# Optimization experiments

Measured on AMD Instinct MI355X. Metric: run time of the kernel, lower is better.

The kernel has to match this reference:

```python
import jax, jax.numpy as jnp
import numpy as np

NUM_HEADS = 8
NEG_INF = float(-2**32 + 1)
LN_EPS = 1e-8


def setup_inputs() -> dict:
    key = jax.random.key(0)
    ks = jax.random.split(key, 9)
    B, T, D = 4, 2048, 512
    inp = {
        "queries": jax.random.normal(ks[0], (B, T, D), jnp.float32),
        "keys": jax.random.normal(ks[1], (B, T, D), jnp.float32),
        "values": jax.random.normal(ks[2], (B, T, D), jnp.float32),
        "Wq": jax.random.normal(ks[3], (D, D), jnp.float32) / np.sqrt(D),
        "bq": jnp.zeros((D,), jnp.float32),
        "Wk": jax.random.normal(ks[4], (D, D), jnp.float32) / np.sqrt(D),
        "bk": jnp.zeros((D,), jnp.float32),
        "Wv": jax.random.normal(ks[5], (D, D), jnp.float32) / np.sqrt(D),
        "bv": jnp.zeros((D,), jnp.float32),
        "gamma": jnp.ones((D,), jnp.float32),
        "beta": jnp.zeros((D,), jnp.float32),
    }
    return inp


def _split_heads(x, h):
    # torch.cat(torch.chunk(x, h, dim=2), dim=0): [B,T,D] -> [h*B, T, D/h], head-major
    B, T, D = x.shape
    return x.reshape(B, T, h, D // h).transpose(2, 0, 1, 3).reshape(h * B, T, D // h)


def _merge_heads(x, h, B):
    # inverse: [h*B, T, dh] -> [B, T, h*dh]
    hB, T, dh = x.shape
    return x.reshape(h, B, T, dh).transpose(1, 2, 0, 3).reshape(B, T, h * dh)


def reference(queries, keys, values, Wq, bq, Wk, bk, Wv, bv, gamma, beta):
    h = NUM_HEADS
    B, Tq, D = queries.shape
    dh = D // h

    Q = jax.nn.relu(queries @ Wq + bq)
    K = jax.nn.relu(keys @ Wk + bk)
    V = jax.nn.relu(values @ Wv + bv)

    Q_ = _split_heads(Q, h)  # [h*B, Tq, dh]
    K_ = _split_heads(K, h)
    V_ = _split_heads(V, h)

    scores = jnp.einsum('bqd,bkd->bqk', Q_, K_) / jnp.sqrt(jnp.float32(dh))  # [h*B, Tq, Tk]

    # key padding mask: zero rows in `keys` get -inf scores
    key_mask = jnp.sign(jnp.abs(jnp.sum(keys, axis=-1)))  # [B, Tk]
    key_mask = jnp.tile(key_mask, (h, 1))  # [h*B, Tk]
    scores = jnp.where(key_mask[:, None, :] == 0.0, NEG_INF, scores)

    attn = jax.nn.softmax(scores, axis=-1)

    # query mask applied multiplicatively post-softmax
    query_mask = jnp.sign(jnp.abs(jnp.sum(queries, axis=-1)))  # [B, Tq]
    query_mask = jnp.tile(query_mask, (h, 1))  # [h*B, Tq]
    attn = attn * query_mask[:, :, None]

    out = jnp.einsum('bqk,bkd->bqd', attn, V_)  # [h*B, Tq, dh]
    out = _merge_heads(out, h, B) + queries  # residual

    # custom LayerNorm: torch.std is unbiased (ddof=1), eps added to std
    mean = out.mean(-1, keepdims=True)
    std = jnp.sqrt(out.var(-1, ddof=1, keepdims=True))
    return gamma * (out - mean) / (std + LN_EPS) + beta
```

## Files before the change

kernel.cpp:

```cpp
#include <hip/hip_runtime.h>


typedef __attribute__((ext_vector_type(8))) __bf16 bf16x8;
typedef __attribute__((ext_vector_type(4))) float f32x4;

#if __has_builtin(__builtin_amdgcn_exp2f)
#define EXP2F __builtin_amdgcn_exp2f
#else
#define EXP2F exp2f
#endif

#define QSCALE (0.125f * 1.4426950408889634f)

__device__ __forceinline__ unsigned short f2bf(float f) {
  return __builtin_bit_cast(unsigned short, (__bf16)f);
}
__device__ __forceinline__ unsigned pk2(float a, float b) {
  return (unsigned)f2bf(a) | ((unsigned)f2bf(b) << 16);
}
__device__ __forceinline__ f32x4 mfma16(bf16x8 a, bf16x8 b, f32x4 c) {
  return __builtin_amdgcn_mfma_f32_16x16x32_bf16(a, b, c, 0, 0, 0);
}
__device__ __forceinline__ bf16x8 ld_bf8(const unsigned short* p) {
  return *(const bf16x8*)p;
}
__device__ __forceinline__ void g2l16(const void* g, void* l) {
  __builtin_amdgcn_global_load_lds(
      (const __attribute__((address_space(1))) void*)g,
      (__attribute__((address_space(3))) void*)l, 16, 0, 0);
}

__global__ __launch_bounds__(256) void wt_kernel(const float* __restrict__ Wq,
                                                 const float* __restrict__ Wk,
                                                 const float* __restrict__ Wv,
                                                 unsigned short* __restrict__ Wt) {
  int idx = blockIdx.x * 256 + threadIdx.x;
  int o = idx * 8;
  int z = o >> 18;
  int rem = o & 262143;
  int n = rem >> 9;
  int k0 = rem & 511;
  const float* W = (z == 0) ? Wq : ((z == 1) ? Wk : Wv);
  unsigned int w[4];
#pragma unroll
  for (int i = 0; i < 4; ++i) {
    unsigned short lo = f2bf(W[(k0 + 2 * i) * 512 + n]);
    unsigned short hi = f2bf(W[(k0 + 2 * i + 1) * 512 + n]);
    w[i] = (unsigned)lo | ((unsigned)hi << 16);
  }
  *(uint4*)(Wt + o) = make_uint4(w[0], w[1], w[2], w[3]);
}

__global__ __launch_bounds__(256, 3) void proj_kernel(
    const float* __restrict__ Xq, const float* __restrict__ Xk,
    const float* __restrict__ Xv, const float* __restrict__ bq,
    const float* __restrict__ bk, const float* __restrict__ bv,
    const unsigned short* __restrict__ Wt, unsigned short* __restrict__ Qb,
    unsigned short* __restrict__ Kb, unsigned short* __restrict__ Vt,
    float* __restrict__ qmask, float* __restrict__ kbias) {
  __shared__ float Asm[128][32];
  __shared__ unsigned short Bsm[128][32];

  int tid = threadIdx.x;
  int m0g = blockIdx.x * 128;
  int z = m0g >> 13;
  int m0 = m0g & 8191;
  int n0 = blockIdx.y * 128;
  const float* X = (z == 0) ? Xq : ((z == 1) ? Xk : Xv);
  const float* bias = (z == 0) ? bq : ((z == 1) ? bk : bv);
  const unsigned short* Wz = Wt + z * 262144;

  int w = tid >> 6, lane = tid & 63;
  int wm = w >> 1, wn = w & 1;
  int mrow = lane & 15, quad = lane >> 4;
  int m7 = mrow & 7;

  int arow = tid >> 3, aslot = tid & 7;
  const float* gA = X + (m0 + arow) * 512 + ((aslot ^ (arow & 7)) * 4);
  char* lA = (char*)&Asm[0][0] + tid * 16;

  int srow = tid >> 2, schk = tid & 3;
  const unsigned short* gB = Wz + (n0 + srow) * 512 + schk * 8;
  char* lB = (char*)&Bsm[0][0] + tid * 16;

  const unsigned short* rB = &Bsm[0][quad * 8];

  f32x4 zero = {0.f, 0.f, 0.f, 0.f};
  f32x4 acc[4][4];
#pragma unroll
  for (int i = 0; i < 4; ++i)
#pragma unroll
    for (int j = 0; j < 4; ++j) acc[i][j] = zero;

  bool domask = (z < 2) && (n0 == 0) && (wn == 0);
  float rsum[4] = {0.f, 0.f, 0.f, 0.f};

  for (int kc = 0; kc < 16; ++kc) {
    int ko = kc * 32;
#pragma unroll
    for (int j = 0; j < 4; ++j) g2l16(gA + ko + j * 32 * 512, lA + j * 4096);
    g2l16(gB + ko, lB);
    g2l16(gB + ko + 64 * 512, lB + 4096);
    __syncthreads();

    bf16x8 af[4], bfr[4];
#pragma unroll
    for (int mt = 0; mt < 4; ++mt) {
      const float* pa = &Asm[wm * 64 + mt * 16 + mrow][0];
      f32x4 lo = *(const f32x4*)(pa + ((2 * quad) ^ m7) * 4);
      f32x4 hi = *(const f32x4*)(pa + ((2 * quad + 1) ^ m7) * 4);
      if (domask)
        rsum[mt] += lo[0] + lo[1] + lo[2] + lo[3] + hi[0] + hi[1] + hi[2] + hi[3];
      bf16x8 t;
      t[0] = (__bf16)lo[0]; t[1] = (__bf16)lo[1];
      t[2] = (__bf16)lo[2]; t[3] = (__bf16)lo[3];
      t[4] = (__bf16)hi[0]; t[5] = (__bf16)hi[1];
      t[6] = (__bf16)hi[2]; t[7] = (__bf16)hi[3];
      af[mt] = t;
    }
#pragma unroll
    for (int nt = 0; nt < 4; ++nt)
      bfr[nt] = ld_bf8(rB + (wn * 64 + nt * 16 + mrow) * 32);
#pragma unroll
    for (int mt = 0; mt < 4; ++mt)
#pragma unroll
      for (int nt = 0; nt < 4; ++nt)
        acc[mt][nt] = mfma16(af[mt], bfr[nt], acc[mt][nt]);
    __syncthreads();
  }

  if (domask) {
    float* msk = (z == 0) ? qmask : kbias;
#pragma unroll
    for (int mt = 0; mt < 4; ++mt) {
      float s = rsum[mt];
      s += __shfl_xor(s, 16);
      s += __shfl_xor(s, 32);
      if (quad == 0) {
        float v;
        if (z == 0)
          v = (s == 0.f) ? 0.f : 1.f;
        else
          v = (s == 0.f) ? -1.0e30f : 0.f;
        msk[m0 + wm * 64 + mt * 16 + mrow] = v;
      }
    }
  }

  if (z < 2) {
    unsigned short* dst = (z == 0) ? Qb : Kb;
    float sc = (z == 0) ? QSCALE : 1.0f;
#pragma unroll
    for (int nt = 0; nt < 4; ++nt) {
      int n = n0 + wn * 64 + nt * 16 + mrow;
      float bv_ = bias[n];
#pragma unroll
      for (int mt = 0; mt < 4; ++mt) {
        int m = m0 + wm * 64 + mt * 16 + quad * 4;
#pragma unroll
        for (int r = 0; r < 4; ++r) {
          float v = fmaxf(acc[mt][nt][r] + bv_, 0.f) * sc;
          dst[(m + r) * 512 + n] = f2bf(v);
        }
      }
    }
  } else {
#pragma unroll
    for (int nt = 0; nt < 4; ++nt) {
      int n = n0 + wn * 64 + nt * 16 + mrow;
      int hh = n >> 6, jj = n & 63;
      float bv_ = bias[n];
#pragma unroll
      for (int mt = 0; mt < 4; ++mt) {
        int grow = m0 + wm * 64 + mt * 16 + quad * 4;
        int bb = grow >> 11, tl = grow & 2047;
        int pos = (tl & ~31) + quad * 8 + (mt & 1) * 4;
        float p0 = fmaxf(acc[mt][nt][0] + bv_, 0.f);
        float p1 = fmaxf(acc[mt][nt][1] + bv_, 0.f);
        float p2 = fmaxf(acc[mt][nt][2] + bv_, 0.f);
        float p3 = fmaxf(acc[mt][nt][3] + bv_, 0.f);
        *(uint2*)(Vt + ((hh * 4 + bb) * 64 + jj) * 2048 + pos) =
            make_uint2(pk2(p0, p1), pk2(p2, p3));
      }
    }
  }
}

__global__ __launch_bounds__(512, 4) void attn_kernel(
    const unsigned short* __restrict__ Qb, const unsigned short* __restrict__ Kb,
    const unsigned short* __restrict__ Vt, const float* __restrict__ qmask,
    const float* __restrict__ kbias, const float* __restrict__ queries,
    float* __restrict__ out) {
  __shared__ char smem[66560];
  unsigned short* KsmS = (unsigned short*)smem;
  unsigned short* VsmS = (unsigned short*)(smem + 32768);
  float* Obuf = (float*)smem;
  float* lbuf = (float*)(smem + 65536);

  int hb = blockIdx.x;
  int qt = blockIdx.y;
  int h = hb >> 2, b = hb & 3;
  int q0 = qt * 128;
  int tid = threadIdx.x;
  int w = tid >> 6, lane = tid & 63;
  int qh = w >> 1, kh2 = w & 1;
  int mrow = lane & 15, quad = lane >> 4;

  const unsigned short* gK =
      Kb + (b * 2048 + (tid >> 3)) * 512 + h * 64 + (((tid & 7) ^ ((tid >> 3) & 7)) * 8);
  const unsigned short* gV =
      Vt + (hb * 64 + (tid >> 4)) * 2048 + (((tid & 15) ^ ((tid >> 4) & 15)) * 8);

  bf16x8 qf[2][2];
  {
    const unsigned short* qp =
        Qb + (b * 2048 + q0 + qh * 32 + mrow) * 512 + h * 64 + quad * 8;
#pragma unroll
    for (int qn = 0; qn < 2; ++qn) {
      qf[qn][0] = ld_bf8(qp + qn * 8192);
      qf[qn][1] = ld_bf8(qp + qn * 8192 + 32);
    }
  }

  bf16x8 onev;
#pragma unroll
  for (int i = 0; i < 8; ++i) onev[i] = (__bf16)1.0f;

  f32x4 zero = {0.f, 0.f, 0.f, 0.f};
  f32x4 oacc[4][2];
#pragma unroll
  for (int i = 0; i < 4; ++i)
#pragma unroll
    for (int j = 0; j < 2; ++j) oacc[i][j] = zero;
  f32x4 lacc[2] = {zero, zero};

  const float* kmB = kbias + b * 2048 + kh2 * 64 + quad * 4;
  const int kfrow = kh2 * 64;
  const int mlow = mrow & 7;

#pragma unroll
  for (int j = 0; j < 2; ++j) {
    g2l16(gK + j * 64 * 512, &KsmS[j * 4096 + tid * 8]);
    g2l16(gV + j * 32 * 2048, &VsmS[j * 4096 + tid * 8]);
  }

  for (int it = 0; it < 16; ++it) {
    int bi = it & 1;
    int kb = it * 128;
    __syncthreads();

    if (it < 15) {
      int nkb = kb + 128;
      int nb = 1 - bi;
#pragma unroll
      for (int j = 0; j < 2; ++j) {
        g2l16(gK + (nkb + j * 64) * 512, &KsmS[nb * 8192 + j * 4096 + tid * 8]);
        g2l16(gV + nkb + j * 32 * 2048, &VsmS[nb * 8192 + j * 4096 + tid * 8]);
      }
    }

    f32x4 kmv[4];
#pragma unroll
    for (int mt = 0; mt < 4; ++mt)
      kmv[mt] = *(const f32x4*)(kmB + kb + mt * 16);

#pragma unroll
    for (int kg = 0; kg < 2; ++kg) {
      bf16x8 kfA0 = ld_bf8(&KsmS[bi * 8192 + (kfrow + kg * 32 + mrow) * 64 +
                                 ((quad) ^ mlow) * 8]);
      bf16x8 kfA1 = ld_bf8(&KsmS[bi * 8192 + (kfrow + kg * 32 + mrow) * 64 +
                                 ((4 + quad) ^ mlow) * 8]);
      bf16x8 kfB0 = ld_bf8(&KsmS[bi * 8192 + (kfrow + kg * 32 + 16 + mrow) * 64 +
                                 ((quad) ^ mlow) * 8]);
      bf16x8 kfB1 = ld_bf8(&KsmS[bi * 8192 + (kfrow + kg * 32 + 16 + mrow) * 64 +
                                 ((4 + quad) ^ mlow) * 8]);
      bf16x8 vfg[4];
#pragma unroll
      for (int dt = 0; dt < 4; ++dt)
        vfg[dt] = ld_bf8(&VsmS[bi * 8192 + (dt * 16 + mrow) * 128 +
                               ((kh2 * 8 + kg * 4 + quad) ^ mrow) * 8]);

      f32x4 sA[2], sB[2];
#pragma unroll
      for (int qn = 0; qn < 2; ++qn) {
        f32x4 s0 = mfma16(kfA0, qf[qn][0], kmv[kg * 2]);
        sA[qn] = mfma16(kfA1, qf[qn][1], s0);
        f32x4 s1 = mfma16(kfB0, qf[qn][0], kmv[kg * 2 + 1]);
        sB[qn] = mfma16(kfB1, qf[qn][1], s1);
      }
#pragma unroll
      for (int qn = 0; qn < 2; ++qn) {
        f32x4 p0, p1;
#pragma unroll
        for (int r = 0; r < 4; ++r) {
          p0[r] = EXP2F(sA[qn][r]);
          p1[r] = EXP2F(sB[qn][r]);
        }
        bf16x8 pf = __builtin_bit_cast(
            bf16x8, make_uint4(pk2(p0[0], p0[1]), pk2(p0[2], p0[3]),
                               pk2(p1[0], p1[1]), pk2(p1[2], p1[3])));
        lacc[qn] = mfma16(pf, onev, lacc[qn]);
#pragma unroll
        for (int dt = 0; dt < 4; ++dt)
          oacc[dt][qn] = mfma16(pf, vfg[dt], oacc[dt][qn]);
      }
    }
  }

  __syncthreads();
  if (mrow == 0) {
#pragma unroll
    for (int qn = 0; qn < 2; ++qn)
#pragma unroll
      for (int r = 0; r < 4; ++r)
        lbuf[kh2 * 128 + qh * 32 + qn * 16 + quad * 4 + r] = lacc[qn][r];
  }
  if (kh2 == 1) {
#pragma unroll
    for (int dt = 0; dt < 4; ++dt)
#pragma unroll
      for (int qn = 0; qn < 2; ++qn)
#pragma unroll
        for (int r = 0; r < 4; ++r)
          Obuf[(qh * 32 + qn * 16 + quad * 4 + r) * 65 + dt * 16 + mrow] =
              oacc[dt][qn][r];
  }
  __syncthreads();
  if (kh2 == 0) {
#pragma unroll
    for (int qn = 0; qn < 2; ++qn) {
#pragma unroll
      for (int r = 0; r < 4; ++r) {
        int qrow = qh * 32 + qn * 16 + quad * 4 + r;
        float l = lbuf[qrow] + lbuf[128 + qrow];
        int qg = b * 2048 + q0 + qrow;
        float inv = qmask[qg] / l;
#pragma unroll
        for (int dt = 0; dt < 4; ++dt) {
          int idx = qg * 512 + h * 64 + dt * 16 + mrow;
          out[idx] =
              (oacc[dt][qn][r] + Obuf[qrow * 65 + dt * 16 + mrow]) * inv +
              queries[idx];
        }
      }
    }
  }
}

__global__ __launch_bounds__(256) void ln_kernel(float* __restrict__ out,
                                                 const float* __restrict__ gamma,
                                                 const float* __restrict__ beta) {
  int row = blockIdx.x * 4 + (threadIdx.x >> 6);
  int lane = threadIdx.x & 63;
  float* p = out + row * 512;
  float4 v1 = ((const float4*)p)[lane];
  float4 v2 = ((const float4*)p)[64 + lane];
  float s = v1.x + v1.y + v1.z + v1.w + v2.x + v2.y + v2.z + v2.w;
  float sq = v1.x * v1.x + v1.y * v1.y + v1.z * v1.z + v1.w * v1.w +
             v2.x * v2.x + v2.y * v2.y + v2.z * v2.z + v2.w * v2.w;
#pragma unroll
  for (int off = 32; off > 0; off >>= 1) {
    s += __shfl_xor(s, off);
    sq += __shfl_xor(sq, off);
  }
  float mean = s * (1.f / 512.f);
  float var = fmaxf((sq - 512.f * mean * mean) * (1.f / 511.f), 0.f);
  float inv = 1.f / (sqrtf(var) + 1e-8f);
  float4 g1 = ((const float4*)gamma)[lane];
  float4 g2 = ((const float4*)gamma)[64 + lane];
  float4 b1 = ((const float4*)beta)[lane];
  float4 b2 = ((const float4*)beta)[64 + lane];
  v1.x = g1.x * (v1.x - mean) * inv + b1.x;
  v1.y = g1.y * (v1.y - mean) * inv + b1.y;
  v1.z = g1.z * (v1.z - mean) * inv + b1.z;
  v1.w = g1.w * (v1.w - mean) * inv + b1.w;
  v2.x = g2.x * (v2.x - mean) * inv + b2.x;
  v2.y = g2.y * (v2.y - mean) * inv + b2.y;
  v2.z = g2.z * (v2.z - mean) * inv + b2.z;
  v2.w = g2.w * (v2.w - mean) * inv + b2.w;
  ((float4*)p)[lane] = v1;
  ((float4*)p)[64 + lane] = v2;
}

extern "C" void kernel_launch(void* const* d_in, const int* in_sizes, int n_in,
                              void* d_out, int out_size, void* d_ws, size_t ws_size,
                              hipStream_t stream) {
  (void)in_sizes; (void)n_in; (void)out_size; (void)ws_size;
  const float* queries = (const float*)d_in[0];
  const float* keys    = (const float*)d_in[1];
  const float* values  = (const float*)d_in[2];
  const float* Wq = (const float*)d_in[3];
  const float* bq = (const float*)d_in[4];
  const float* Wk = (const float*)d_in[5];
  const float* bk = (const float*)d_in[6];
  const float* Wv = (const float*)d_in[7];
  const float* bv = (const float*)d_in[8];
  const float* gamma = (const float*)d_in[9];
  const float* beta  = (const float*)d_in[10];
  float* out = (float*)d_out;

  char* ws = (char*)d_ws;
  unsigned short* Qb = (unsigned short*)(ws);
  unsigned short* Kb = (unsigned short*)(ws + 8 * 1024 * 1024);
  unsigned short* Vt = (unsigned short*)(ws + 16 * 1024 * 1024);
  unsigned short* Wt = (unsigned short*)(ws + 24 * 1024 * 1024);
  float* qmask = (float*)(ws + 24 * 1024 * 1024 + 3 * 512 * 512 * 2);
  float* kbias = qmask + 8192;

  wt_kernel<<<384, 256, 0, stream>>>(Wq, Wk, Wv, Wt);
  proj_kernel<<<dim3(192, 4), 256, 0, stream>>>(queries, keys, values, bq, bk, bv,
                                                Wt, Qb, Kb, Vt, qmask, kbias);
  attn_kernel<<<dim3(32, 16), 512, 0, stream>>>(Qb, Kb, Vt, qmask, kbias, queries, out);
  ln_kernel<<<2048, 256, 0, stream>>>(out, gamma, beta);
}
```

Before: 193.4 us.

## Pre-convert inputs to bf16, double-buffer projection GEMM, shrink attention tiles

Adds a separate kernel that converts the Q/K/V inputs to bf16 and computes the query and key masks, so the projection GEMM loads bf16 tiles with double-buffered LDS prefetch and no longer converts or reduces per tile. The attention kernel moves to 256 threads and 64 query rows per block, doubling the grid. It reads V fragments straight from global memory instead of staging them in LDS, and replaces the ones-vector MFMA row-sum with scalar adds plus shuffles. The trade-offs are an extra kernel launch and an extra round trip of the inputs through memory (partly staged in the output buffer), plus uncoalesced global V loads in the inner loop.

```diff
diff --git a/kernel.cpp b/kernel.cpp
--- a/kernel.cpp
+++ b/kernel.cpp
@@ -51,39 +51,66 @@
   *(uint4*)(Wt + o) = make_uint4(w[0], w[1], w[2], w[3]);
 }
 
-__global__ __launch_bounds__(256, 3) void proj_kernel(
+__global__ __launch_bounds__(256) void xcvt_kernel(
     const float* __restrict__ Xq, const float* __restrict__ Xk,
-    const float* __restrict__ Xv, const float* __restrict__ bq,
+    const float* __restrict__ Xv, unsigned short* __restrict__ Xbq,
+    unsigned short* __restrict__ Xbk, unsigned short* __restrict__ Xbv,
+    float* __restrict__ qmask, float* __restrict__ kbias) {
+  int row = blockIdx.x * 4 + (threadIdx.x >> 6);
+  int lane = threadIdx.x & 63;
+  int z = row >> 13;
+  int r = row & 8191;
+  const float* X = (z == 0) ? Xq : ((z == 1) ? Xk : Xv);
+  unsigned short* Xb = (z == 0) ? Xbq : ((z == 1) ? Xbk : Xbv);
+  const float* p = X + r * 512 + lane * 8;
+  f32x4 lo = *(const f32x4*)p;
+  f32x4 hi = *(const f32x4*)(p + 4);
+  *(uint4*)(Xb + r * 512 + lane * 8) =
+      make_uint4(pk2(lo[0], lo[1]), pk2(lo[2], lo[3]), pk2(hi[0], hi[1]),
+                 pk2(hi[2], hi[3]));
+  if (z < 2) {
+    float s = lo[0] + lo[1] + lo[2] + lo[3] + hi[0] + hi[1] + hi[2] + hi[3];
+#pragma unroll
+    for (int off = 1; off < 64; off <<= 1) s += __shfl_xor(s, off);
+    if (lane == 0) {
+      if (z == 0)
+        qmask[r] = (s == 0.f) ? 0.f : 1.f;
+      else
+        kbias[r] = (s == 0.f) ? -1.0e30f : 0.f;
+    }
+  }
+}
+
+__global__ __launch_bounds__(256, 4) void proj_kernel(
+    const unsigned short* __restrict__ Xbq, const unsigned short* __restrict__ Xbk,
+    const unsigned short* __restrict__ Xbv, const float* __restrict__ bq,
     const float* __restrict__ bk, const float* __restrict__ bv,
     const unsigned short* __restrict__ Wt, unsigned short* __restrict__ Qb,
-    unsigned short* __restrict__ Kb, unsigned short* __restrict__ Vt,
-    float* __restrict__ qmask, float* __restrict__ kbias) {
-  __shared__ float Asm[128][32];
-  __shared__ unsigned short Bsm[128][32];
+    unsigned short* __restrict__ Kb, unsigned short* __restrict__ Vt) {
+  __shared__ unsigned short Asm[2][128][32];
+  __shared__ unsigned short Bsm[2][128][32];
 
   int tid = threadIdx.x;
   int m0g = blockIdx.x * 128;
   int z = m0g >> 13;
   int m0 = m0g & 8191;
   int n0 = blockIdx.y * 128;
-  const float* X = (z == 0) ? Xq : ((z == 1) ? Xk : Xv);
+  const unsigned short* Xb = (z == 0) ? Xbq : ((z == 1) ? Xbk : Xbv);
   const float* bias = (z == 0) ? bq : ((z == 1) ? bk : bv);
   const unsigned short* Wz = Wt + z * 262144;
 
   int w = tid >> 6, lane = tid & 63;
   int wm = w >> 1, wn = w & 1;
   int mrow = lane & 15, quad = lane >> 4;
-  int m7 = mrow & 7;
-
-  int arow = tid >> 3, aslot = tid & 7;
-  const float* gA = X + (m0 + arow) * 512 + ((aslot ^ (arow & 7)) * 4);
-  char* lA = (char*)&Asm[0][0] + tid * 16;
-
-  int srow = tid >> 2, schk = tid & 3;
-  const unsigned short* gB = Wz + (n0 + srow) * 512 + schk * 8;
-  char* lB = (char*)&Bsm[0][0] + tid * 16;
-
-  const unsigned short* rB = &Bsm[0][quad * 8];
+
+  int srow = tid >> 2, sslot = tid & 3;
+  int sxs = sslot ^ ((srow >> 1) & 3);
+  const unsigned short* gA = Xb + (m0 + srow) * 512 + sxs * 8;
+  const unsigned short* gB = Wz + (n0 + srow) * 512 + sxs * 8;
+  char* lA = (char*)&Asm[0][0][0] + tid * 16;
+  char* lB = (char*)&Bsm[0][0][0] + tid * 16;
+
+  int rs = (quad ^ ((mrow >> 1) & 3)) * 8;
 
   f32x4 zero = {0.f, 0.f, 0.f, 0.f};
   f32x4 acc[4][4];
@@ -92,59 +119,35 @@
 #pragma unroll
     for (int j = 0; j < 4; ++j) acc[i][j] = zero;
 
-  bool domask = (z < 2) && (n0 == 0) && (wn == 0);
-  float rsum[4] = {0.f, 0.f, 0.f, 0.f};
+  g2l16(gA, lA);
+  g2l16(gA + 64 * 512, lA + 4096);
+  g2l16(gB, lB);
+  g2l16(gB + 64 * 512, lB + 4096);
+  __syncthreads();
 
   for (int kc = 0; kc < 16; ++kc) {
-    int ko = kc * 32;
-#pragma unroll
-    for (int j = 0; j < 4; ++j) g2l16(gA + ko + j * 32 * 512, lA + j * 4096);
-    g2l16(gB + ko, lB);
-    g2l16(gB + ko + 64 * 512, lB + 4096);
-    __syncthreads();
-
+    int cur = kc & 1;
+    if (kc < 15) {
+      int ko = (kc + 1) * 32;
+      int nb = cur ^ 1;
+      g2l16(gA + ko, lA + nb * 8192);
+      g2l16(gA + ko + 64 * 512, lA + nb * 8192 + 4096);
+      g2l16(gB + ko, lB + nb * 8192);
+      g2l16(gB + ko + 64 * 512, lB + nb * 8192 + 4096);
+    }
     bf16x8 af[4], bfr[4];
 #pragma unroll
-    for (int mt = 0; mt < 4; ++mt) {
-      const float* pa = &Asm[wm * 64 + mt * 16 + mrow][0];
-      f32x4 lo = *(const f32x4*)(pa + ((2 * quad) ^ m7) * 4);
-      f32x4 hi = *(const f32x4*)(pa + ((2 * quad + 1) ^ m7) * 4);
-      if (domask)
-        rsum[mt] += lo[0] + lo[1] + lo[2] + lo[3] + hi[0] + hi[1] + hi[2] + hi[3];
-      bf16x8 t;
-      t[0] = (__bf16)lo[0]; t[1] = (__bf16)lo[1];
-      t[2] = (__bf16)lo[2]; t[3] = (__bf16)lo[3];
-      t[4] = (__bf16)hi[0]; t[5] = (__bf16)hi[1];
-      t[6] = (__bf16)hi[2]; t[7] = (__bf16)hi[3];
-      af[mt] = t;
-    }
+    for (int mt = 0; mt < 4; ++mt)
+      af[mt] = ld_bf8(&Asm[cur][wm * 64 + mt * 16 + mrow][rs]);
 #pragma unroll
     for (int nt = 0; nt < 4; ++nt)
-      bfr[nt] = ld_bf8(rB + (wn * 64 + nt * 16 + mrow) * 32);
+      bfr[nt] = ld_bf8(&Bsm[cur][wn * 64 + nt * 16 + mrow][rs]);
 #pragma unroll
     for (int mt = 0; mt < 4; ++mt)
 #pragma unroll
       for (int nt = 0; nt < 4; ++nt)
         acc[mt][nt] = mfma16(af[mt], bfr[nt], acc[mt][nt]);
     __syncthreads();
-  }
-
-  if (domask) {
-    float* msk = (z == 0) ? qmask : kbias;
-#pragma unroll
-    for (int mt = 0; mt < 4; ++mt) {
-      float s = rsum[mt];
-      s += __shfl_xor(s, 16);
-      s += __shfl_xor(s, 32);
-      if (quad == 0) {
-        float v;
-        if (z == 0)
-          v = (s == 0.f) ? 0.f : 1.f;
-        else
-          v = (s == 0.f) ? -1.0e30f : 0.f;
-        msk[m0 + wm * 64 + mt * 16 + mrow] = v;
-      }
-    }
   }
 
   if (z < 2) {
@@ -186,30 +189,30 @@
   }
 }
 
-__global__ __launch_bounds__(512, 4) void attn_kernel(
+__global__ __launch_bounds__(256, 4) void attn_kernel(
     const unsigned short* __restrict__ Qb, const unsigned short* __restrict__ Kb,
     const unsigned short* __restrict__ Vt, const float* __restrict__ qmask,
     const float* __restrict__ kbias, const float* __restrict__ queries,
     float* __restrict__ out) {
-  __shared__ char smem[66560];
+  __shared__ char smem[33280];
   unsigned short* KsmS = (unsigned short*)smem;
-  unsigned short* VsmS = (unsigned short*)(smem + 32768);
   float* Obuf = (float*)smem;
-  float* lbuf = (float*)(smem + 65536);
+  float* lbuf = (float*)(smem + 32768);
 
   int hb = blockIdx.x;
   int qt = blockIdx.y;
   int h = hb >> 2, b = hb & 3;
-  int q0 = qt * 128;
+  int q0 = qt * 64;
   int tid = threadIdx.x;
   int w = tid >> 6, lane = tid & 63;
   int qh = w >> 1, kh2 = w & 1;
   int mrow = lane & 15, quad = lane >> 4;
+  int mlow = mrow & 7;
 
   const unsigned short* gK =
       Kb + (b * 2048 + (tid >> 3)) * 512 + h * 64 + (((tid & 7) ^ ((tid >> 3) & 7)) * 8);
   const unsigned short* gV =
-      Vt + (hb * 64 + (tid >> 4)) * 2048 + (((tid & 15) ^ ((tid >> 4) & 15)) * 8);
+      Vt + (hb * 64 + mrow) * 2048 + (kh2 * 8 + quad) * 8;
 
   bf16x8 qf[2][2];
   {
@@ -222,27 +225,20 @@
     }
   }
 
-  bf16x8 onev;
-#pragma unroll
-  for (int i = 0; i < 8; ++i) onev[i] = (__bf16)1.0f;
-
   f32x4 zero = {0.f, 0.f, 0.f, 0.f};
   f32x4 oacc[4][2];
 #pragma unroll
   for (int i = 0; i < 4; ++i)
 #pragma unroll
     for (int j = 0; j < 2; ++j) oacc[i][j] = zero;
-  f32x4 lacc[2] = {zero, zero};
+  float lpart[2] = {0.f, 0.f};
 
   const float* kmB = kbias + b * 2048 + kh2 * 64 + quad * 4;
   const int kfrow = kh2 * 64;
-  const int mlow = mrow & 7;
-
-#pragma unroll
-  for (int j = 0; j < 2; ++j) {
-    g2l16(gK + j * 64 * 512, &KsmS[j * 4096 + tid * 8]);
-    g2l16(gV + j * 32 * 2048, &VsmS[j * 4096 + tid * 8]);
-  }
+
+#pragma unroll
+  for (int j = 0; j < 4; ++j)
+    g2l16(gK + j * 32 * 512, &KsmS[j * 2048 + tid * 8]);
 
   for (int it = 0; it < 16; ++it) {
     int bi = it & 1;
@@ -250,22 +246,16 @@
     __syncthreads();
 
     if (it < 15) {
-      int nkb = kb + 128;
       int nb = 1 - bi;
 #pragma unroll
-      for (int j = 0; j < 2; ++j) {
-        g2l16(gK + (nkb + j * 64) * 512, &KsmS[nb * 8192 + j * 4096 + tid * 8]);
-        g2l16(gV + nkb + j * 32 * 2048, &VsmS[nb * 8192 + j * 4096 + tid * 8]);
-      }
-    }
-
-    f32x4 kmv[4];
-#pragma unroll
-    for (int mt = 0; mt < 4; ++mt)
-      kmv[mt] = *(const f32x4*)(kmB + kb + mt * 16);
+      for (int j = 0; j < 4; ++j)
+        g2l16(gK + (kb + 128 + j * 32) * 512, &KsmS[nb * 8192 + j * 2048 + tid * 8]);
+    }
 
 #pragma unroll
     for (int kg = 0; kg < 2; ++kg) {
+      f32x4 km0 = *(const f32x4*)(kmB + kb + kg * 32);
+      f32x4 km1 = *(const f32x4*)(kmB + kb + kg * 32 + 16);
       bf16x8 kfA0 = ld_bf8(&KsmS[bi * 8192 + (kfrow + kg * 32 + mrow) * 64 +
                                  ((quad) ^ mlow) * 8]);
       bf16x8 kfA1 = ld_bf8(&KsmS[bi * 8192 + (kfrow + kg * 32 + mrow) * 64 +
@@ -277,15 +267,14 @@
       bf16x8 vfg[4];
 #pragma unroll
       for (int dt = 0; dt < 4; ++dt)
-        vfg[dt] = ld_bf8(&VsmS[bi * 8192 + (dt * 16 + mrow) * 128 +
-                               ((kh2 * 8 + kg * 4 + quad) ^ mrow) * 8]);
+        vfg[dt] = ld_bf8(gV + dt * 16 * 2048 + kb + kg * 32);
 
       f32x4 sA[2], sB[2];
 #pragma unroll
       for (int qn = 0; qn < 2; ++qn) {
-        f32x4 s0 = mfma16(kfA0, qf[qn][0], kmv[kg * 2]);
+        f32x4 s0 = mfma16(kfA0, qf[qn][0], km0);
         sA[qn] = mfma16(kfA1, qf[qn][1], s0);
-        f32x4 s1 = mfma16(kfB0, qf[qn][0], kmv[kg * 2 + 1]);
+        f32x4 s1 = mfma16(kfB0, qf[qn][0], km1);
         sB[qn] = mfma16(kfB1, qf[qn][1], s1);
       }
 #pragma unroll
@@ -296,10 +285,10 @@
           p0[r] = EXP2F(sA[qn][r]);
           p1[r] = EXP2F(sB[qn][r]);
         }
+        lpart[qn] += p0[0] + p0[1] + p0[2] + p0[3] + p1[0] + p1[1] + p1[2] + p1[3];
         bf16x8 pf = __builtin_bit_cast(
             bf16x8, make_uint4(pk2(p0[0], p0[1]), pk2(p0[2], p0[3]),
                                pk2(p1[0], p1[1]), pk2(p1[2], p1[3])));
-        lacc[qn] = mfma16(pf, onev, lacc[qn]);
 #pragma unroll
         for (int dt = 0; dt < 4; ++dt)
           oacc[dt][qn] = mfma16(pf, vfg[dt], oacc[dt][qn]);
@@ -307,13 +296,16 @@
     }
   }
 
+#pragma unroll
+  for (int qn = 0; qn < 2; ++qn) {
+    lpart[qn] += __shfl_xor(lpart[qn], 16);
+    lpart[qn] += __shfl_xor(lpart[qn], 32);
+  }
   __syncthreads();
-  if (mrow == 0) {
+  if (quad == 0) {
 #pragma unroll
     for (int qn = 0; qn < 2; ++qn)
-#pragma unroll
-      for (int r = 0; r < 4; ++r)
-        lbuf[kh2 * 128 + qh * 32 + qn * 16 + quad * 4 + r] = lacc[qn][r];
+      lbuf[kh2 * 64 + qh * 32 + qn * 16 + mrow] = lpart[qn];
   }
   if (kh2 == 1) {
 #pragma unroll
@@ -332,7 +324,7 @@
 #pragma unroll
       for (int r = 0; r < 4; ++r) {
         int qrow = qh * 32 + qn * 16 + quad * 4 + r;
-        float l = lbuf[qrow] + lbuf[128 + qrow];
+        float l = lbuf[qrow] + lbuf[64 + qrow];
         int qg = b * 2048 + q0 + qrow;
         float inv = qmask[qg] / l;
 #pragma unroll
@@ -404,12 +396,19 @@
   unsigned short* Kb = (unsigned short*)(ws + 8 * 1024 * 1024);
   unsigned short* Vt = (unsigned short*)(ws + 16 * 1024 * 1024);
   unsigned short* Wt = (unsigned short*)(ws + 24 * 1024 * 1024);
-  float* qmask = (float*)(ws + 24 * 1024 * 1024 + 3 * 512 * 512 * 2);
+  unsigned short* Xbv = (unsigned short*)(ws + 26 * 1024 * 1024);
+  float* qmask = (float*)(ws + 34 * 1024 * 1024);
   float* kbias = qmask + 8192;
 
+  unsigned short* Xbq = (unsigned short*)d_out;
+  unsigned short* Xbk = Xbq + 4194304;
+
   wt_kernel<<<384, 256, 0, stream>>>(Wq, Wk, Wv, Wt);
-  proj_kernel<<<dim3(192, 4), 256, 0, stream>>>(queries, keys, values, bq, bk, bv,
-                                                Wt, Qb, Kb, Vt, qmask, kbias);
-  attn_kernel<<<dim3(32, 16), 512, 0, stream>>>(Qb, Kb, Vt, qmask, kbias, queries, out);
+  xcvt_kernel<<<6144, 256, 0, stream>>>(queries, keys, values, Xbq, Xbk, Xbv,
+                                        qmask, kbias);
+  proj_kernel<<<dim3(192, 4), 256, 0, stream>>>(Xbq, Xbk, Xbv, bq, bk, bv,
+                                                Wt, Qb, Kb, Vt);
+  attn_kernel<<<dim3(32, 32), 256, 0, stream>>>(Qb, Kb, Vt, qmask, kbias,
+                                                queries, out);
   ln_kernel<<<2048, 256, 0, stream>>>(out, gamma, beta);
 }
```

Result: slower. 250.0 us (+29.3%).
